# Performance work log

Hardware: AMD Instinct MI355X
Metric: run time of the kernel (lower is better)

The kernel has to match this reference:

```python
import jax, jax.numpy as jnp
import numpy as np

NH = 12      # attention heads
EPS = 1e-5   # torch nn.LayerNorm default


def _ln(x, g, b):
    m = jnp.mean(x, axis=-1, keepdims=True)
    v = jnp.var(x, axis=-1, keepdims=True)
    return (x - m) * jax.lax.rsqrt(v + EPS) * g + b


def _rel_table(table, n):
    # q_size == k_size == n, table length == 2n-1 -> pure gather, no interpolation
    idx = jnp.arange(n)[:, None] - jnp.arange(n)[None, :] + (n - 1)
    return table[idx]  # (n, n, head_dim)


def _attn2d(x, qkv_w, qkv_b, proj_w, proj_b, rel_h, rel_w):
    B, H, W, C = x.shape
    hd = C // NH
    scale = hd ** -0.5
    N = H * W
    qkv = x.reshape(B, N, C) @ qkv_w + qkv_b                    # (B, N, 3C)
    qkv = qkv.reshape(B, N, 3, NH, hd).transpose(2, 0, 3, 1, 4).reshape(3, B * NH, N, hd)
    q, k, v = qkv[0], qkv[1], qkv[2]
    attn = jnp.einsum('bnd,bmd->bnm', q * scale, k)             # (B*NH, N, N)
    Rh = _rel_table(rel_h, H)
    Rw = _rel_table(rel_w, W)
    rq = q.reshape(B * NH, H, W, hd)                            # unscaled q, as in torch
    bias_h = jnp.einsum('bhwc,hkc->bhwk', rq, Rh)
    bias_w = jnp.einsum('bhwc,wkc->bhwk', rq, Rw)
    attn = (attn.reshape(B * NH, H, W, H, W)
            + bias_h[:, :, :, :, None]
            + bias_w[:, :, :, None, :]).reshape(B * NH, N, N)
    attn = jax.nn.softmax(attn, axis=-1)
    out = (attn @ v).reshape(B, NH, H, W, hd).transpose(0, 2, 3, 1, 4).reshape(B, H, W, C)
    return out @ proj_w + proj_b


def _win_part(x, ws):
    B, H, W, C = x.shape
    ph = (ws - H % ws) % ws
    pw = (ws - W % ws) % ws
    x = jnp.pad(x, ((0, 0), (0, ph), (0, pw), (0, 0)))
    Hp, Wp = H + ph, W + pw
    x = x.reshape(B, Hp // ws, ws, Wp // ws, ws, C).transpose(0, 1, 3, 2, 4, 5)
    return x.reshape(-1, ws, ws, C), (Hp, Wp)


def _win_unpart(wins, ws, pad_hw, hw):
    Hp, Wp = pad_hw
    H, W = hw
    B = wins.shape[0] // (Hp * Wp // ws // ws)
    x = wins.reshape(B, Hp // ws, Wp // ws, ws, ws, -1).transpose(0, 1, 3, 2, 4, 5)
    x = x.reshape(B, Hp, Wp, -1)
    return x[:, :H, :W, :]


def _block(x, ws, ln1g, ln1b, qkvw, qkvb, projw, projb, relh, relw,
           ln2g, ln2b, mw1, mb1, mw2, mb2):
    shortcut = x
    x = _ln(x, ln1g, ln1b)
    if ws > 0:
        H, W = x.shape[1], x.shape[2]
        x, pad_hw = _win_part(x, ws)
    x = _attn2d(x, qkvw, qkvb, projw, projb, relh, relw)
    if ws > 0:
        x = _win_unpart(x, ws, pad_hw, (H, W))
    x = shortcut + x
    h = _ln(x, ln2g, ln2b)
    h = jax.nn.gelu(h @ mw1 + mb1, approximate=False) @ mw2 + mb2
    return x + h


def setup_inputs() -> dict:
    key = jax.random.key(0)
    def rnd(i, shape, s=0.02):
        return jax.random.normal(jax.random.fold_in(key, i), shape, jnp.float32) * s
    C, M, HD = 768, 3072, 64
    d = {
        'x': rnd(0, (1, 3, 1024, 1024), 1.0),
        'patch_w': rnd(1, (16, 16, 3, C)),
        'patch_b': rnd(2, (C,)),
        'pos_embed': rnd(3, (1, 64, 64, C)),
    }
    i = 4
    for s, L in (('1', 27), ('2', 127)):
        for name, shape in (('ln1g', (C,)), ('ln1b', (C,)), ('qkvw', (C, 3 * C)),
                            ('qkvb', (3 * C,)), ('projw', (C, C)), ('projb', (C,)),
                            ('relh', (L, HD)), ('relw', (L, HD)),
                            ('ln2g', (C,)), ('ln2b', (C,)),
                            ('mw1', (C, M)), ('mb1', (M,)), ('mw2', (M, C)), ('mb2', (C,))):
            d[name + s] = rnd(i, shape)
            i += 1
    for s in ('1', '2'):
        d['ln1g' + s] = d['ln1g' + s] + 1.0
        d['ln2g' + s] = d['ln2g' + s] + 1.0
    return d


def reference(x, patch_w, patch_b, pos_embed,
              ln1g1, ln1b1, qkvw1, qkvb1, projw1, projb1, relh1, relw1,
              ln2g1, ln2b1, mw11, mb11, mw21, mb21,
              ln1g2, ln1b2, qkvw2, qkvb2, projw2, projb2, relh2, relw2,
              ln2g2, ln2b2, mw12, mb12, mw22, mb22):
    # patch embed: 16x16 stride-16 conv, output NHWC (B, 64, 64, 768)
    feat = jax.lax.conv_general_dilated(
        x, patch_w, window_strides=(16, 16), padding='VALID',
        dimension_numbers=('NCHW', 'HWIO', 'NHWC'))
    feat = feat + patch_b + pos_embed
    feat = _block(feat, 14, ln1g1, ln1b1, qkvw1, qkvb1, projw1, projb1,
                  relh1, relw1, ln2g1, ln2b1, mw11, mb11, mw21, mb21)
    feat = _block(feat, 0, ln1g2, ln1b2, qkvw2, qkvb2, projw2, projb2,
                  relh2, relw2, ln2g2, ln2b2, mw12, mb12, mw22, mb22)
    return feat
```

## Files before the change

### kernel.cpp

```cpp
#include <hip/hip_runtime.h>


using u16 = unsigned short;
using u32 = unsigned int;
using short8  = __attribute__((ext_vector_type(8))) short;
using floatx4 = __attribute__((ext_vector_type(4))) float;

__device__ __forceinline__ float bfu2f(u16 u) { return __builtin_bit_cast(float, (u32)u << 16); }
__device__ __forceinline__ u16   f2bfu(float f) {
  u32 u = __builtin_bit_cast(u32, f);
  return (u16)((u + 0x7fffu + ((u >> 16) & 1u)) >> 16);
}
__device__ __forceinline__ u32 cvtpk_bf16(float a, float b) {
  u32 r; asm("v_cvt_pk_bf16_f32 %0, %1, %2" : "=v"(r) : "v"(a), "v"(b)); return r;
}
#define DIV14(x) (((x) * 4682) >> 16)
#define WAIT_VM0()   __builtin_amdgcn_s_waitcnt(0x3f70)
#define WAIT_LGKM0() __builtin_amdgcn_s_waitcnt(0xc07f)

__device__ __forceinline__ void gld_lds16(const u16* g, u16* l) {
  __builtin_amdgcn_global_load_lds(
      (const __attribute__((address_space(1))) u32*)g,
      (__attribute__((address_space(3))) u32*)l, 16, 0, 0);
}

__global__ __launch_bounds__(256) void detect_k(const u16* __restrict__ x, int* __restrict__ flag)
{
  __shared__ int tot;
  if (threadIdx.x == 0) tot = 0;
  __syncthreads();
  int cnt = 0;
  for (int i = threadIdx.x; i < 4096; i += 256) {
    int e = (x[2 * i] >> 7) & 0xFF;
    cnt += (e >= 100 && e <= 134) ? 1 : 0;
  }
  atomicAdd(&tot, cnt);
  __syncthreads();
  if (threadIdx.x == 0) *flag = (tot >= 2458) ? 1 : 0;
}

struct CvtEnt { const void* src; int n; int dstoff; };
struct CvtArgs { CvtEnt e[24]; int cnt; };

__global__ __launch_bounds__(256) void tobf_multi_k(CvtArgs a, u16* __restrict__ dst,
                                                    const int* __restrict__ flag)
{
  int gid = blockIdx.x * 256 + threadIdx.x;
  bool isbf = (*flag != 0);
  for (int t = 0; t < a.cnt; ++t)
    if (gid < a.e[t].n)
      dst[a.e[t].dstoff + gid] = isbf ? ((const u16*)a.e[t].src)[gid]
                                      : f2bfu(((const float*)a.e[t].src)[gid]);
}

__global__ __launch_bounds__(256) void tobf4_k(const void* __restrict__ src, u16* __restrict__ dst,
                                               int n4, const int* __restrict__ flag)
{
  int i = blockIdx.x * 256 + threadIdx.x;
  if (i >= n4) return;
  ushort4 o;
  if (*flag) o = ((const ushort4*)src)[i];
  else {
    float4 f = ((const float4*)src)[i];
    o.x = f2bfu(f.x); o.y = f2bfu(f.y); o.z = f2bfu(f.z); o.w = f2bfu(f.w);
  }
  ((ushort4*)dst)[i] = o;
}

__global__ __launch_bounds__(256) void cvt_out_k(const float* __restrict__ src,
                                                 void* __restrict__ dst,
                                                 const int* __restrict__ flag)
{
  int i = blockIdx.x * 256 + threadIdx.x;
  float4 v = ((const float4*)src)[i];
  if (*flag) {
    ushort4 o;
    o.x = f2bfu(v.x); o.y = f2bfu(v.y); o.z = f2bfu(v.z); o.w = f2bfu(v.w);
    ((ushort4*)dst)[i] = o;
  } else {
    ((float4*)dst)[i] = v;
  }
}

struct TJob { const void* src; int dstoff; int K; int N; int blk0; };
struct TArgs { TJob j[6]; int njobs; };

__global__ __launch_bounds__(256) void tobfT_multi_k(TArgs a, u16* __restrict__ wa,
                                                     const int* __restrict__ flag)
{
  __shared__ u16 t[64][65];
  const int bid = blockIdx.x;
  int ji = 0;
  #pragma unroll
  for (int q = 1; q < 6; ++q) if (q < a.njobs && bid >= a.j[q].blk0) ji = q;
  const void* src = a.j[ji].src;
  u16* dst = wa + a.j[ji].dstoff;
  const int K = a.j[ji].K, N = a.j[ji].N;
  const int local = bid - a.j[ji].blk0;
  const int nx = N >> 6;
  const int bx = local % nx, by = local / nx;
  const int n0 = bx * 64, k0 = by * 64;
  const int r = threadIdx.x >> 2, c = (threadIdx.x & 3) * 16;
  if (*flag) {
    const u16* s = (const u16*)src + (size_t)(k0 + r) * N + n0 + c;
    union { uint4 v[2]; u16 e[16]; } u;
    u.v[0] = *(const uint4*)s; u.v[1] = *(const uint4*)(s + 8);
    #pragma unroll
    for (int j = 0; j < 16; ++j) t[c + j][r] = u.e[j];
  } else {
    const float* s = (const float*)src + (size_t)(k0 + r) * N + n0 + c;
    #pragma unroll
    for (int j = 0; j < 16; ++j) t[c + j][r] = f2bfu(s[j]);
  }
  __syncthreads();
  union { uint4 v[2]; u16 e[16]; } o;
  #pragma unroll
  for (int j = 0; j < 16; ++j) o.e[j] = t[r][c + j];
  u16* d = dst + (size_t)(n0 + r) * K + k0 + c;
  *(uint4*)d = o.v[0]; *(uint4*)(d + 8) = o.v[1];
}

__global__ __launch_bounds__(256) void im2col_k(const void* __restrict__ xv, u16* __restrict__ a,
                                                const int* __restrict__ flag)
{
  int t = blockIdx.x, tid = threadIdx.x;
  int py = t >> 6, px = t & 63;
  int ky = tid >> 4, kx = tid & 15;
  size_t src = (size_t)(py * 16 + ky) * 1024 + px * 16 + kx;
  u16 v0, v1, v2;
  if (*flag) {
    const u16* x = (const u16*)xv;
    v0 = x[src]; v1 = x[src + 1048576]; v2 = x[src + 2097152];
  } else {
    const float* x = (const float*)xv;
    v0 = f2bfu(x[src]); v1 = f2bfu(x[src + 1048576]); v2 = f2bfu(x[src + 2097152]);
  }
  size_t dst = (size_t)t * 768 + tid * 3;
  a[dst] = v0; a[dst + 1] = v1; a[dst + 2] = v2;
}

__global__ __launch_bounds__(256) void ln_k(const float* __restrict__ x,
                                            const u16* __restrict__ g,
                                            const u16* __restrict__ b,
                                            u16* __restrict__ y)
{
  const int t = blockIdx.x, tid = threadIdx.x;
  const float* xp = x + (size_t)t * 768;
  float v0 = xp[tid], v1 = xp[tid + 256], v2 = xp[tid + 512];
  float s = v0 + v1 + v2;
  float q = v0 * v0 + v1 * v1 + v2 * v2;
  #pragma unroll
  for (int off = 32; off; off >>= 1) { s += __shfl_xor(s, off); q += __shfl_xor(q, off); }
  __shared__ float red[8];
  int wid = tid >> 6, lane = tid & 63;
  if (lane == 0) { red[wid] = s; red[4 + wid] = q; }
  __syncthreads();
  s = red[0] + red[1] + red[2] + red[3];
  q = red[4] + red[5] + red[6] + red[7];
  float mean = s * (1.f / 768.f);
  float var  = q * (1.f / 768.f) - mean * mean;
  float rstd = rsqrtf(var + 1e-5f);
  u16* yp = y + (size_t)t * 768;
  yp[tid]       = f2bfu((v0 - mean) * rstd * bfu2f(g[tid])       + bfu2f(b[tid]));
  yp[tid + 256] = f2bfu((v1 - mean) * rstd * bfu2f(g[tid + 256]) + bfu2f(b[tid + 256]));
  yp[tid + 512] = f2bfu((v2 - mean) * rstd * bfu2f(g[tid + 512]) + bfu2f(b[tid + 512]));
}

__global__ __launch_bounds__(256) void ln_win_k(const float* __restrict__ x,
                                                const u16* __restrict__ g,
                                                const u16* __restrict__ b,
                                                u16* __restrict__ wout)
{
  const int t = blockIdx.x, tid = threadIdx.x;
  const int win = t / 196, tok = t - win * 196;
  const int ty = DIV14(tok), tx = tok - 14 * ty;
  const int gy = (win / 5) * 14 + ty, gx = (win % 5) * 14 + tx;
  u16* yp = wout + (size_t)t * 768;
  if (gy >= 64 || gx >= 64) {
    yp[tid] = 0; yp[tid + 256] = 0; yp[tid + 512] = 0;
    return;
  }
  const float* xp = x + (size_t)(gy * 64 + gx) * 768;
  float v0 = xp[tid], v1 = xp[tid + 256], v2 = xp[tid + 512];
  float s = v0 + v1 + v2;
  float q = v0 * v0 + v1 * v1 + v2 * v2;
  #pragma unroll
  for (int off = 32; off; off >>= 1) { s += __shfl_xor(s, off); q += __shfl_xor(q, off); }
  __shared__ float red[8];
  int wid = tid >> 6, lane = tid & 63;
  if (lane == 0) { red[wid] = s; red[4 + wid] = q; }
  __syncthreads();
  s = red[0] + red[1] + red[2] + red[3];
  q = red[4] + red[5] + red[6] + red[7];
  float mean = s * (1.f / 768.f);
  float var  = q * (1.f / 768.f) - mean * mean;
  float rstd = rsqrtf(var + 1e-5f);
  yp[tid]       = f2bfu((v0 - mean) * rstd * bfu2f(g[tid])       + bfu2f(b[tid]));
  yp[tid + 256] = f2bfu((v1 - mean) * rstd * bfu2f(g[tid + 256]) + bfu2f(b[tid + 256]));
  yp[tid + 512] = f2bfu((v2 - mean) * rstd * bfu2f(g[tid + 512]) + bfu2f(b[tid + 512]));
}

enum { MODE_QKV = 1, MODE_GELU = 3, MODE_FEATA = 5, MODE_RESA = 6 };

template<int BN>
__global__ __launch_bounds__(256) void mgemm_k(
    const u16* __restrict__ A, const u16* __restrict__ Bt, const u16* __restrict__ bias,
    int M, int N, int K, int mode,
    float* __restrict__ outf, u16* __restrict__ outb,
    const float* __restrict__ res, const u16* __restrict__ pos,
    u16* __restrict__ qb, u16* __restrict__ kb, u16* __restrict__ vt, int TW, int TP,
    const int* __restrict__ flagp)
{
  constexpr int NWN = BN / 64, NWM = 4 / NWN;
  constexpr int WTM = 128 / NWM;
  constexpr int MS = WTM / 16, NS = 4;
  __shared__ __align__(16) u16 As[2][128 * 32];
  __shared__ __align__(16) u16 Bs[2][BN * 32];
  const int tid = threadIdx.x;
  const int wid = tid >> 6, lane = tid & 63;
  const int l15 = lane & 15, quad = lane >> 4;
  const int wm = wid / NWN, wn = wid % NWN;
  const int m0 = blockIdx.y * 128, n0 = blockIdx.x * BN;
  const int nz = (int)gridDim.z;
  const int kloc = K / nz;
  const int kbeg = blockIdx.z * kloc, kend = kbeg + kloc;
  const bool z0 = (blockIdx.z == 0);

  floatx4 acc[MS][NS];
  #pragma unroll
  for (int i = 0; i < MS; ++i)
    #pragma unroll
    for (int j = 0; j < NS; ++j) acc[i][j] = (floatx4){0.f, 0.f, 0.f, 0.f};

  const int sr = lane >> 2, sc = (lane & 3) * 8;
  const u16* ag0 = A + (size_t)min(m0 + wid * 32 + sr,      M - 1) * K + sc;
  const u16* ag1 = A + (size_t)min(m0 + wid * 32 + 16 + sr, M - 1) * K + sc;
  const u16 *bg0 = nullptr, *bg1 = nullptr;
  if constexpr (BN == 128) {
    bg0 = Bt + (size_t)(n0 + wid * 32 + sr) * K + sc;
    bg1 = Bt + (size_t)(n0 + wid * 32 + 16 + sr) * K + sc;
  } else {
    bg0 = Bt + (size_t)(n0 + wid * 16 + sr) * K + sc;
  }

  auto issue = [&](int buf, int k0) {
    gld_lds16(ag0 + k0, &As[buf][(wid * 32) * 32]);
    gld_lds16(ag1 + k0, &As[buf][(wid * 32 + 16) * 32]);
    if constexpr (BN == 128) {
      gld_lds16(bg0 + k0, &Bs[buf][(wid * 32) * 32]);
      gld_lds16(bg1 + k0, &Bs[buf][(wid * 32 + 16) * 32]);
    } else {
      gld_lds16(bg0 + k0, &Bs[buf][(wid * 16) * 32]);
    }
  };

  issue(0, kbeg);
  int bufi = 0;
  for (int k0 = kbeg; k0 < kend; k0 += 32, bufi ^= 1) {
    WAIT_VM0();
    __syncthreads();
    if (k0 + 32 < kend) issue(bufi ^ 1, k0 + 32);
    short8 af[MS], bf[NS];
    #pragma unroll
    for (int ms = 0; ms < MS; ++ms)
      af[ms] = *(const short8*)&As[bufi][(wm * WTM + ms * 16 + l15) * 32 + quad * 8];
    #pragma unroll
    for (int ns = 0; ns < NS; ++ns)
      bf[ns] = *(const short8*)&Bs[bufi][(wn * 64 + ns * 16 + l15) * 32 + quad * 8];
    #pragma unroll
    for (int ms = 0; ms < MS; ++ms)
      #pragma unroll
      for (int ns = 0; ns < NS; ++ns)
        acc[ms][ns] = __builtin_amdgcn_mfma_f32_16x16x32_bf16(af[ms], bf[ns], acc[ms][ns], 0, 0, 0);
  }

  #pragma unroll
  for (int ms = 0; ms < MS; ++ms) {
    const int gmb = m0 + wm * WTM + ms * 16 + quad * 4;
    #pragma unroll
    for (int ns = 0; ns < NS; ++ns) {
      const int gn = n0 + wn * 64 + ns * 16 + l15;
      const float bb = bfu2f(bias[gn]);
      if (mode == MODE_QKV) {
        const int s = gn / 768, nn = gn - s * 768, h = nn >> 6, d = nn & 63;
        #pragma unroll
        for (int r = 0; r < 4; ++r) {
          int gm = gmb + r; if (gm >= M) continue;
          float v = acc[ms][ns][r] + bb;
          int b = gm / TW, tok = gm - b * TW;
          size_t bh = (size_t)(b * 12 + h);
          if (s == 0)      qb[(bh * TP + tok) * 64 + d] = f2bfu(v);
          else if (s == 1) kb[(bh * TP + tok) * 64 + d] = f2bfu(v);
          else             vt[(bh * 64 + d) * TP + tok] = f2bfu(v);
        }
      } else if (mode == MODE_GELU) {
        #pragma unroll
        for (int r = 0; r < 4; ++r) {
          int gm = gmb + r; if (gm >= M) continue;
          size_t o = (size_t)gm * N + gn;
          float v = acc[ms][ns][r] + bb;
          outb[o] = f2bfu(0.5f * v * (1.f + erff(v * 0.70710678f)));
        }
      } else if (mode == MODE_FEATA) {
        #pragma unroll
        for (int r = 0; r < 4; ++r) {
          int gm = gmb + r; if (gm >= M) continue;
          size_t o = (size_t)gm * N + gn;
          float v = acc[ms][ns][r];
          if (z0) v += bb + bfu2f(pos[o]);
          unsafeAtomicAdd(&outf[o], v);
        }
      } else {
        #pragma unroll
        for (int r = 0; r < 4; ++r) {
          int gm = gmb + r; if (gm >= M) continue;
          size_t o = (size_t)gm * N + gn;
          float v = acc[ms][ns][r];
          if (z0) v += bb + res[o];
          unsafeAtomicAdd(&outf[o], v);
        }
      }
    }
  }
}

template<int NT, int NTP, int TD, bool WIN>
__global__ __launch_bounds__(256) void flash_k(
    const u16* __restrict__ qb, const u16* __restrict__ kb, const u16* __restrict__ vt,
    const u16* __restrict__ relh, const u16* __restrict__ relw,
    u16* __restrict__ outb)
{
  constexpr int NTAB = 2 * TD - 1;
  constexpr int KT = NTP >> 6;
  constexpr float L2E = 1.4426950408889634f;
  constexpr float SC2 = 0.125f * L2E;
  constexpr int RQ  = 0;
  constexpr int RK0 = 4096;
  constexpr int RK1 = 8192;
  constexpr int RV0 = 12288;
  constexpr int RV1 = 16384;
  constexpr int RG  = 20480;
  constexpr int GWWIN = RG + 64 * 34;
  constexpr int TOT = WIN ? (GWWIN + 64 * 34) : (RG + 64 * 66);
  __shared__ __align__(16) u16 lds[TOT];

  const int tid = threadIdx.x, wid = tid >> 6, lane = tid & 63;
  const int l15 = lane & 15, quad = lane >> 4;
  const int qt = blockIdx.x, bh = blockIdx.y;
  const int q0 = qt * 64;
  const size_t kvbase = (size_t)bh * NTP * 64;
  const size_t vbase  = (size_t)bh * 64 * NTP;
  const int myrow = wid * 16 + l15;

  auto swb = [](int row, int blk) { return row * 64 + (((blk ^ row) & 7) << 3); };

  {
    const int r = tid >> 2, cb = (tid & 3) * 2;
    const int tok = WIN ? (q0 + r) : min(q0 + r, NT - 1);
    const uint4* p = (const uint4*)(qb + kvbase + (size_t)tok * 64 + cb * 8);
    *(uint4*)&lds[RQ + swb(r, cb)]     = p[0];
    *(uint4*)&lds[RQ + swb(r, cb + 1)] = p[1];
  }
  __syncthreads();
  short8 qf[2];
  qf[0] = *(const short8*)&lds[RQ + swb(myrow, quad)];
  qf[1] = *(const short8*)&lds[RQ + swb(myrow, 4 + quad)];
  WAIT_LGKM0();

  auto stageRB = [&](const u16* tab, int rowoff, int maxrow) {
    const int r = tid >> 2, cb = (tid & 3) * 2;
    const int tr = min(rowoff + r, maxrow);
    const uint4* p = (const uint4*)(tab + (size_t)tr * 64 + cb * 8);
    *(uint4*)&lds[RV0 + swb(r, cb)]     = p[0];
    *(uint4*)&lds[RV0 + swb(r, cb + 1)] = p[1];
  };
  auto gpass = [&](int gbase, int gstride, int ncols) {
    for (int ns = 0; ns < ncols / 16; ++ns) {
      floatx4 g = (floatx4){0.f, 0.f, 0.f, 0.f};
      #pragma unroll
      for (int ks = 0; ks < 2; ++ks) {
        short8 b = *(const short8*)&lds[RV0 + swb(ns * 16 + l15, ks * 4 + quad)];
        g = __builtin_amdgcn_mfma_f32_16x16x32_bf16(qf[ks], b, g, 0, 0, 0);
      }
      #pragma unroll
      for (int r = 0; r < 4; ++r)
        lds[gbase + (wid * 16 + quad * 4 + r) * gstride + ns * 16 + l15] = f2bfu(g[r] * L2E);
    }
  };

  float gwv[4][4];
  if constexpr (!WIN) {
    stageRB(relh, qt, NTAB - 1);  __syncthreads();
    gpass(RG, 66, 64);
    __syncthreads();
    stageRB(relw, 0, NTAB - 1);   __syncthreads();
    gpass(RK0, 66, 64);
    #pragma unroll
    for (int kbi = 0; kbi < 4; ++kbi)
      #pragma unroll
      for (int r = 0; r < 4; ++r) {
        const int iw = myrow + 63 - (kbi * 16 + quad * 4 + r);
        if (iw < 64) gwv[kbi][r] = bfu2f(lds[RK0 + myrow * 66 + iw]);
      }
    WAIT_LGKM0();
    __syncthreads();
    stageRB(relw, 64, NTAB - 1);  __syncthreads();
    gpass(RK0, 66, 64);
    #pragma unroll
    for (int kbi = 0; kbi < 4; ++kbi)
      #pragma unroll
      for (int r = 0; r < 4; ++r) {
        const int iw = myrow + 63 - (kbi * 16 + quad * 4 + r);
        if (iw >= 64) gwv[kbi][r] = bfu2f(lds[RK0 + myrow * 66 + iw - 64]);
      }
    WAIT_LGKM0();
  } else {
    stageRB(relh, 0, NTAB - 1);  __syncthreads();
    gpass(RG, 34, 32);
    __syncthreads();
    stageRB(relw, 0, NTAB - 1);  __syncthreads();
    gpass(GWWIN, 34, 32);
  }

  const int srow = lane >> 3;
  const int scol = (((lane & 7) ^ srow) & 7) << 3;
  const u16* kp  = kb + kvbase + (size_t)(wid * 16 + srow) * 64 + scol;
  const u16* kp2 = kp + 512;
  const u16* vp  = vt + vbase  + (size_t)(wid * 16 + srow) * NTP + scol;
  const u16* vp2 = vp + (size_t)8 * NTP;
  u16* const kd0 = &lds[RK0 + wid * 1024];
  u16* const kd1 = &lds[RK1 + wid * 1024];
  u16* const vd0 = &lds[RV0 + wid * 1024];
  u16* const vd1 = &lds[RV1 + wid * 1024];
  auto issueKV = [&](int buf) {
    u16* kdb = buf ? kd1 : kd0;
    u16* vdb = buf ? vd1 : vd0;
    gld_lds16(kp,  kdb);
    gld_lds16(kp2, kdb + 512);
    gld_lds16(vp,  vdb);
    gld_lds16(vp2, vdb + 512);
    kp += 4096; kp2 += 4096; vp += 64; vp2 += 64;
  };

  float mI = -3e38f, lI = 0.f;
  floatx4 Oacc[4];
  #pragma unroll
  for (int d = 0; d < 4; ++d) Oacc[d] = (floatx4){0.f, 0.f, 0.f, 0.f};

  int qy = 0, qx = 0;
  if constexpr (WIN) {
    const int tok0 = q0 + myrow;
    qy = DIV14(tok0); qx = tok0 - 14 * qy;
  }

  auto body = [&](int RKb, int RVb, int kt) {
    floatx4 sacc[4];
    #pragma unroll
    for (int kbi = 0; kbi < 4; ++kbi) sacc[kbi] = (floatx4){0.f, 0.f, 0.f, 0.f};
    __builtin_amdgcn_s_setprio(1);
    #pragma unroll
    for (int ks = 0; ks < 2; ++ks)
      #pragma unroll
      for (int kbi = 0; kbi < 4; ++kbi) {
        short8 a = *(const short8*)&lds[RKb + swb(kbi * 16 + l15, ks * 4 + quad)];
        sacc[kbi] = __builtin_amdgcn_mfma_f32_16x16x32_bf16(a, qf[ks], sacc[kbi], 0, 0, 0);
      }
    __builtin_amdgcn_s_setprio(0);

    float sv[4][4];
    if constexpr (!WIN) {
      #pragma unroll
      for (int kbi = 0; kbi < 4; ++kbi)
        #pragma unroll
        for (int r = 0; r < 4; ++r)
          sv[kbi][r] = fmaf(SC2, sacc[kbi][r], gwv[kbi][r]);
    } else {
      #pragma unroll
      for (int kbi = 0; kbi < 4; ++kbi)
        #pragma unroll
        for (int r = 0; r < 4; ++r) {
          const int j = kt * 64 + kbi * 16 + quad * 4 + r;
          const int ky = DIV14(j), kx = j - 14 * ky;
          int ih = qy - ky + 13; ih = max(0, min(ih, 31));
          int iw = qx - kx + 13; iw = max(0, min(iw, 31));
          float s = SC2 * sacc[kbi][r] + bfu2f(lds[RG + myrow * 34 + ih])
                                       + bfu2f(lds[GWWIN + myrow * 34 + iw]);
          sv[kbi][r] = (j < NT) ? s : -1e30f;
        }
    }

    float rm;
    {
      float a0 = fmaxf(fmaxf(sv[0][0], sv[0][1]), fmaxf(sv[0][2], sv[0][3]));
      float a1 = fmaxf(fmaxf(sv[1][0], sv[1][1]), fmaxf(sv[1][2], sv[1][3]));
      float a2 = fmaxf(fmaxf(sv[2][0], sv[2][1]), fmaxf(sv[2][2], sv[2][3]));
      float a3 = fmaxf(fmaxf(sv[3][0], sv[3][1]), fmaxf(sv[3][2], sv[3][3]));
      rm = fmaxf(fmaxf(a0, a1), fmaxf(a2, a3));
    }
    rm = fmaxf(rm, __shfl_xor(rm, 16));
    rm = fmaxf(rm, __shfl_xor(rm, 32));
    float ghv = 0.f;
    if constexpr (!WIN) ghv = bfu2f(lds[RG + myrow * 66 + (63 - kt)]);
    const float mt = rm + ghv;
    const float mn = fmaxf(mI, mt);
    const float tt = mn - ghv;

    float rs = 0.f;
    u32 pk[8];
    #pragma unroll
    for (int kbi = 0; kbi < 4; ++kbi) {
      float p0 = __builtin_amdgcn_exp2f(sv[kbi][0] - tt);
      float p1 = __builtin_amdgcn_exp2f(sv[kbi][1] - tt);
      float p2 = __builtin_amdgcn_exp2f(sv[kbi][2] - tt);
      float p3 = __builtin_amdgcn_exp2f(sv[kbi][3] - tt);
      rs += (p0 + p1) + (p2 + p3);
      pk[2 * kbi]     = cvtpk_bf16(p0, p1);
      pk[2 * kbi + 1] = cvtpk_bf16(p2, p3);
    }

    #pragma unroll
    for (int kbi = 0; kbi < 4; ++kbi) {
      const int col = kbi * 16 + quad * 4;
      uint2 w2; w2.x = pk[2 * kbi]; w2.y = pk[2 * kbi + 1];
      *(uint2*)&lds[RQ + myrow * 64 + ((((col >> 3) ^ myrow) & 7) << 3) + (col & 7)] = w2;
    }

    const float al = __builtin_amdgcn_exp2f(mI - mn);
    if (__any(mt > mI)) {
      #pragma unroll
      for (int d = 0; d < 4; ++d) Oacc[d] *= al;
    }
    mI = mn;

    __builtin_amdgcn_s_setprio(1);
    #pragma unroll
    for (int ks = 0; ks < 2; ++ks) {
      short8 pb = *(const short8*)&lds[RQ + swb(myrow, ks * 4 + quad)];
      #pragma unroll
      for (int d = 0; d < 4; ++d) {
        short8 a = *(const short8*)&lds[RVb + swb(d * 16 + l15, ks * 4 + quad)];
        Oacc[d] = __builtin_amdgcn_mfma_f32_16x16x32_bf16(a, pb, Oacc[d], 0, 0, 0);
      }
    }
    __builtin_amdgcn_s_setprio(0);

    rs += __shfl_xor(rs, 16);
    rs += __shfl_xor(rs, 32);
    lI = fmaf(lI, al, rs);
  };

  __syncthreads();
  issueKV(0);
  for (int kt = 0; kt < KT; kt += 2) {
    WAIT_VM0();
    __syncthreads();
    if (kt + 1 < KT) issueKV(1);
    body(RK0, RV0, kt);
    WAIT_VM0();
    __syncthreads();
    if (kt + 2 < KT) issueKV(0);
    body(RK1, RV1, kt + 1);
  }

  const float rinv = 1.f / lI;
  const int tok = q0 + myrow;
  u32 ow[8];
  #pragma unroll
  for (int d = 0; d < 4; ++d) {
    ow[2 * d]     = cvtpk_bf16(Oacc[d][0] * rinv, Oacc[d][1] * rinv);
    ow[2 * d + 1] = cvtpk_bf16(Oacc[d][2] * rinv, Oacc[d][3] * rinv);
  }
  if constexpr (WIN) {
    if (tok < NT) {
      const int win = bh / 12, h = bh - win * 12;
      const int ty = DIV14(tok), tx = tok - 14 * ty;
      const int gy = (win / 5) * 14 + ty, gx = (win % 5) * 14 + tx;
      if (gy < 64 && gx < 64) {
        u16* op = outb + (size_t)(gy * 64 + gx) * 768 + h * 64;
        #pragma unroll
        for (int d = 0; d < 4; ++d)
          *(uint2*)(op + d * 16 + quad * 4) = make_uint2(ow[2 * d], ow[2 * d + 1]);
      }
    }
  } else {
    u16* op = outb + (size_t)tok * 768 + bh * 64;
    #pragma unroll
    for (int d = 0; d < 4; ++d)
      *(uint2*)(op + d * 16 + quad * 4) = make_uint2(ow[2 * d], ow[2 * d + 1]);
  }
}

extern "C" void kernel_launch(void* const* d_in, const int* in_sizes, int n_in,
                              void* d_out, int out_size, void* d_ws, size_t ws_size,
                              hipStream_t stream)
{
  const void* x      = d_in[0];
  const void* patchw = d_in[1];
  const void* patchb = d_in[2];
  const void* pos    = d_in[3];
  const void *ln1g1 = d_in[4],  *ln1b1 = d_in[5];
  const void *qkvw1 = d_in[6],  *qkvb1 = d_in[7];
  const void *projw1= d_in[8],  *projb1= d_in[9];
  const void *relh1 = d_in[10], *relw1 = d_in[11];
  const void *ln2g1 = d_in[12], *ln2b1 = d_in[13];
  const void *mw11  = d_in[14], *mb11  = d_in[15];
  const void *mw21  = d_in[16], *mb21  = d_in[17];
  const void *ln1g2 = d_in[18], *ln1b2 = d_in[19];
  const void *qkvw2 = d_in[20], *qkvb2 = d_in[21];
  const void *projw2= d_in[22], *projb2= d_in[23];
  const void *relh2 = d_in[24], *relw2 = d_in[25];
  const void *ln2g2 = d_in[26], *ln2b2 = d_in[27];
  const void *mw12  = d_in[28], *mb12  = d_in[29];
  const void *mw22  = d_in[30], *mb22  = d_in[31];

  char* w = (char*)d_ws;
  int*   FLAG = (int*)w;  w += 64;
  float* R0 = (float*)w;  w += 12582912;
  float* R1 = (float*)w;  w += 12582912;
  u16*   B0 = (u16*)w;    w += 6291456;
  u16*   Wb = (u16*)w;    w += 7526400;
  u16*   QB = (u16*)w;    w += 9830400;
  u16*   KB = (u16*)w;    w += 9830400;
  u16*   VT = (u16*)w;    w += 9830400;
  u16*   Hb = (u16*)w;    w += 25165824;
  u16*   WA = (u16*)w;    w += 15335424;
  u16*   POSb = (u16*)w;  w += 6291456;
  u16*   PRM = (u16*)w;   w += 106560;
  u16*   Ap = Hb;

  constexpr int WA_QKV = 0, WA_PROJ = 1769472, WA_M1 = 2359296, WA_M2 = 4718592,
                WA_PATCH = 7077888;
  constexpr int PRM_PATCHB = 0, PB1 = 768, PBLK = 26240, PB2 = 768 + PBLK;
  constexpr int O_QKVB = 0, O_PROJB = 2304, O_MB1 = 3072, O_MB2 = 6144,
                O_LN1G = 6912, O_LN1B = 7680, O_LN2G = 8448, O_LN2B = 9216,
                O_RELH = 9984, O_RELW = 18112;

  detect_k<<<1, 256, 0, stream>>>((const u16*)x, FLAG);
  CvtArgs ca; int kk = 0;
  auto add = [&](const void* s, int n, int off) { ca.e[kk].src = s; ca.e[kk].n = n; ca.e[kk].dstoff = off; ++kk; };
  add(patchb, 768, PRM_PATCHB);
  add(qkvb1, 2304, PB1 + O_QKVB); add(projb1, 768, PB1 + O_PROJB);
  add(mb11, 3072, PB1 + O_MB1);   add(mb21, 768, PB1 + O_MB2);
  add(ln1g1, 768, PB1 + O_LN1G);  add(ln1b1, 768, PB1 + O_LN1B);
  add(ln2g1, 768, PB1 + O_LN2G);  add(ln2b1, 768, PB1 + O_LN2B);
  add(relh1, 27 * 64, PB1 + O_RELH); add(relw1, 27 * 64, PB1 + O_RELW);
  add(qkvb2, 2304, PB2 + O_QKVB); add(projb2, 768, PB2 + O_PROJB);
  add(mb12, 3072, PB2 + O_MB1);   add(mb22, 768, PB2 + O_MB2);
  add(ln1g2, 768, PB2 + O_LN1G);  add(ln1b2, 768, PB2 + O_LN1B);
  add(ln2g2, 768, PB2 + O_LN2G);  add(ln2b2, 768, PB2 + O_LN2B);
  add(relh2, 127 * 64, PB2 + O_RELH); add(relw2, 127 * 64, PB2 + O_RELW);
  ca.cnt = kk;
  tobf_multi_k<<<32, 256, 0, stream>>>(ca, PRM, FLAG);
  tobf4_k<<<3072, 256, 0, stream>>>(pos, POSb, 786432, FLAG);

  {
    TArgs ta; int nb = 0, jn = 0;
    auto addT = [&](const void* s, int dstoff, int K, int N) {
      ta.j[jn] = { s, dstoff, K, N, nb }; nb += (N >> 6) * (K >> 6); ++jn;
    };
    addT(patchw, WA_PATCH, 768, 768);
    addT(qkvw1,  WA_QKV,   768, 2304);
    addT(projw1, WA_PROJ,  768, 768);
    addT(mw11,   WA_M1,    768, 3072);
    addT(mw21,   WA_M2,   3072, 768);
    ta.njobs = jn;
    tobfT_multi_k<<<nb, 256, 0, stream>>>(ta, WA, FLAG);
  }

  im2col_k<<<4096, 256, 0, stream>>>(x, Ap, FLAG);
  hipMemsetAsync(R0, 0, 12582912, stream);
  mgemm_k<64><<<dim3(12, 32, 2), 256, 0, stream>>>(Ap, WA + WA_PATCH, PRM + PRM_PATCHB,
      4096, 768, 768, MODE_FEATA, R0, nullptr, nullptr, POSb, nullptr, nullptr, nullptr, 0, 0, FLAG);

  ln_win_k<<<4900, 256, 0, stream>>>(R0, PRM + PB1 + O_LN1G, PRM + PB1 + O_LN1B, Wb);
  hipMemsetAsync(VT, 0, 9830400, stream);
  mgemm_k<128><<<dim3(18, 39), 256, 0, stream>>>(Wb, WA + WA_QKV, PRM + PB1 + O_QKVB,
      4900, 2304, 768, MODE_QKV, nullptr, nullptr, nullptr, nullptr, QB, KB, VT, 196, 256, FLAG);
  flash_k<196, 256, 14, true><<<dim3(4, 300), 256, 0, stream>>>(QB, KB, VT,
      PRM + PB1 + O_RELH, PRM + PB1 + O_RELW, B0);
  hipMemsetAsync(R1, 0, 12582912, stream);
  mgemm_k<64><<<dim3(12, 32, 2), 256, 0, stream>>>(B0, WA + WA_PROJ, PRM + PB1 + O_PROJB,
      4096, 768, 768, MODE_RESA, R1, nullptr, R0, nullptr, nullptr, nullptr, nullptr, 0, 0, FLAG);
  ln_k<<<4096, 256, 0, stream>>>(R1, PRM + PB1 + O_LN2G, PRM + PB1 + O_LN2B, B0);
  mgemm_k<128><<<dim3(24, 32), 256, 0, stream>>>(B0, WA + WA_M1, PRM + PB1 + O_MB1,
      4096, 3072, 768, MODE_GELU, nullptr, Hb, nullptr, nullptr, nullptr, nullptr, nullptr, 0, 0, FLAG);
  hipMemsetAsync(R0, 0, 12582912, stream);
  mgemm_k<64><<<dim3(12, 32, 2), 256, 0, stream>>>(Hb, WA + WA_M2, PRM + PB1 + O_MB2,
      4096, 768, 3072, MODE_RESA, R0, nullptr, R1, nullptr, nullptr, nullptr, nullptr, 0, 0, FLAG);

  {
    TArgs ta; int nb = 0, jn = 0;
    auto addT = [&](const void* s, int dstoff, int K, int N) {
      ta.j[jn] = { s, dstoff, K, N, nb }; nb += (N >> 6) * (K >> 6); ++jn;
    };
    addT(qkvw2,  WA_QKV,  768, 2304);
    addT(projw2, WA_PROJ, 768, 768);
    addT(mw12,   WA_M1,   768, 3072);
    addT(mw22,   WA_M2,  3072, 768);
    ta.njobs = jn;
    tobfT_multi_k<<<nb, 256, 0, stream>>>(ta, WA, FLAG);
  }

  ln_k<<<4096, 256, 0, stream>>>(R0, PRM + PB2 + O_LN1G, PRM + PB2 + O_LN1B, B0);
  mgemm_k<128><<<dim3(18, 32), 256, 0, stream>>>(B0, WA + WA_QKV, PRM + PB2 + O_QKVB,
      4096, 2304, 768, MODE_QKV, nullptr, nullptr, nullptr, nullptr, QB, KB, VT, 4096, 4096, FLAG);
  flash_k<4096, 4096, 64, false><<<dim3(64, 12), 256, 0, stream>>>(QB, KB, VT,
      PRM + PB2 + O_RELH, PRM + PB2 + O_RELW, B0);
  hipMemsetAsync(R1, 0, 12582912, stream);
  mgemm_k<64><<<dim3(12, 32, 2), 256, 0, stream>>>(B0, WA + WA_PROJ, PRM + PB2 + O_PROJB,
      4096, 768, 768, MODE_RESA, R1, nullptr, R0, nullptr, nullptr, nullptr, nullptr, 0, 0, FLAG);
  ln_k<<<4096, 256, 0, stream>>>(R1, PRM + PB2 + O_LN2G, PRM + PB2 + O_LN2B, B0);
  mgemm_k<128><<<dim3(24, 32), 256, 0, stream>>>(B0, WA + WA_M1, PRM + PB2 + O_MB1,
      4096, 3072, 768, MODE_GELU, nullptr, Hb, nullptr, nullptr, nullptr, nullptr, nullptr, 0, 0, FLAG);
  hipMemsetAsync(R0, 0, 12582912, stream);
  mgemm_k<64><<<dim3(12, 32, 2), 256, 0, stream>>>(Hb, WA + WA_M2, PRM + PB2 + O_MB2,
      4096, 768, 3072, MODE_RESA, R0, nullptr, R1, nullptr, nullptr, nullptr, nullptr, 0, 0, FLAG);
  cvt_out_k<<<3072, 256, 0, stream>>>(R0, d_out, FLAG);
}
```

Measured before the change: 788.8 us.

## Replace split-K atomic GEMMs with dedicated 64x64 swizzled-LDS GEMM kernel

Result: faster. 712.6 us (-9.7%).

```diff
diff --git a/kernel.cpp b/kernel.cpp
--- a/kernel.cpp
+++ b/kernel.cpp
@@ -65,21 +65,6 @@
     o.x = f2bfu(f.x); o.y = f2bfu(f.y); o.z = f2bfu(f.z); o.w = f2bfu(f.w);
   }
   ((ushort4*)dst)[i] = o;
-}
-
-__global__ __launch_bounds__(256) void cvt_out_k(const float* __restrict__ src,
-                                                 void* __restrict__ dst,
-                                                 const int* __restrict__ flag)
-{
-  int i = blockIdx.x * 256 + threadIdx.x;
-  float4 v = ((const float4*)src)[i];
-  if (*flag) {
-    ushort4 o;
-    o.x = f2bfu(v.x); o.y = f2bfu(v.y); o.z = f2bfu(v.z); o.w = f2bfu(v.w);
-    ((ushort4*)dst)[i] = o;
-  } else {
-    ((float4*)dst)[i] = v;
-  }
 }
 
 struct TJob { const void* src; int dstoff; int K; int N; int blk0; };
@@ -200,14 +185,89 @@
   yp[tid + 512] = f2bfu((v2 - mean) * rstd * bfu2f(g[tid + 512]) + bfu2f(b[tid + 512]));
 }
 
-enum { MODE_QKV = 1, MODE_GELU = 3, MODE_FEATA = 5, MODE_RESA = 6 };
+enum { MODE_FEAT = 0, MODE_QKV = 1, MODE_RES = 2, MODE_GELU = 3, MODE_OUT = 4 };
+
+__global__ __launch_bounds__(256) void mgemm64_k(
+    const u16* __restrict__ A, const u16* __restrict__ Bt, const u16* __restrict__ bias,
+    int N, int K, int mode,
+    float* __restrict__ outf, u16* __restrict__ outb,
+    const float* __restrict__ res, const u16* __restrict__ pos,
+    const int* __restrict__ flagp)
+{
+  __shared__ __align__(16) u16 As[2][64 * 64];
+  __shared__ __align__(16) u16 Bs[2][64 * 64];
+  const int tid = threadIdx.x;
+  const int wid = tid >> 6, lane = tid & 63;
+  const int l15 = lane & 15, quad = lane >> 4;
+  const int m0 = blockIdx.y * 64, n0 = blockIdx.x * 64;
+
+  auto swb = [](int row, int blk) { return row * 64 + (((blk ^ row) & 7) << 3); };
+
+  floatx4 acc[4];
+  #pragma unroll
+  for (int ns = 0; ns < 4; ++ns) acc[ns] = (floatx4){0.f, 0.f, 0.f, 0.f};
+
+  const int srow = lane >> 3;
+  const int scol = ((lane & 7) ^ srow) << 3;
+  const u16* ap0 = A  + (size_t)(m0 + wid * 16 + srow) * K + scol;
+  const u16* ap1 = ap0 + (size_t)8 * K;
+  const u16* bp0 = Bt + (size_t)(n0 + wid * 16 + srow) * K + scol;
+  const u16* bp1 = bp0 + (size_t)8 * K;
+
+  auto issue = [&](int buf, int k0) {
+    gld_lds16(ap0 + k0, &As[buf][(wid * 16) * 64]);
+    gld_lds16(ap1 + k0, &As[buf][(wid * 16 + 8) * 64]);
+    gld_lds16(bp0 + k0, &Bs[buf][(wid * 16) * 64]);
+    gld_lds16(bp1 + k0, &Bs[buf][(wid * 16 + 8) * 64]);
+  };
+
+  issue(0, 0);
+  int bufi = 0;
+  for (int k0 = 0; k0 < K; k0 += 64, bufi ^= 1) {
+    WAIT_VM0();
+    __syncthreads();
+    if (k0 + 64 < K) issue(bufi ^ 1, k0 + 64);
+    short8 af[2], bf[4][2];
+    af[0] = *(const short8*)&As[bufi][swb(wid * 16 + l15, quad)];
+    af[1] = *(const short8*)&As[bufi][swb(wid * 16 + l15, 4 + quad)];
+    #pragma unroll
+    for (int ns = 0; ns < 4; ++ns) {
+      bf[ns][0] = *(const short8*)&Bs[bufi][swb(ns * 16 + l15, quad)];
+      bf[ns][1] = *(const short8*)&Bs[bufi][swb(ns * 16 + l15, 4 + quad)];
+    }
+    #pragma unroll
+    for (int ns = 0; ns < 4; ++ns) {
+      acc[ns] = __builtin_amdgcn_mfma_f32_16x16x32_bf16(af[0], bf[ns][0], acc[ns], 0, 0, 0);
+      acc[ns] = __builtin_amdgcn_mfma_f32_16x16x32_bf16(af[1], bf[ns][1], acc[ns], 0, 0, 0);
+    }
+  }
+
+  const bool outbf = (mode == MODE_OUT) ? (*flagp != 0) : false;
+  const int gm0 = m0 + wid * 16 + quad * 4;
+  #pragma unroll
+  for (int ns = 0; ns < 4; ++ns) {
+    const int gn = n0 + ns * 16 + l15;
+    const float bb = bfu2f(bias[gn]);
+    #pragma unroll
+    for (int r = 0; r < 4; ++r) {
+      const size_t o = (size_t)(gm0 + r) * N + gn;
+      float v = acc[ns][r] + bb;
+      if (mode == MODE_FEAT)      outf[o] = v + bfu2f(pos[o]);
+      else if (mode == MODE_RES)  outf[o] = v + res[o];
+      else {
+        float ov = v + res[o];
+        if (outbf) outb[o] = f2bfu(ov);
+        else       outf[o] = ov;
+      }
+    }
+  }
+}
 
 template<int BN>
 __global__ __launch_bounds__(256) void mgemm_k(
     const u16* __restrict__ A, const u16* __restrict__ Bt, const u16* __restrict__ bias,
     int M, int N, int K, int mode,
-    float* __restrict__ outf, u16* __restrict__ outb,
-    const float* __restrict__ res, const u16* __restrict__ pos,
+    u16* __restrict__ outb,
     u16* __restrict__ qb, u16* __restrict__ kb, u16* __restrict__ vt, int TW, int TP,
     const int* __restrict__ flagp)
 {
@@ -221,10 +281,6 @@
   const int l15 = lane & 15, quad = lane >> 4;
   const int wm = wid / NWN, wn = wid % NWN;
   const int m0 = blockIdx.y * 128, n0 = blockIdx.x * BN;
-  const int nz = (int)gridDim.z;
-  const int kloc = K / nz;
-  const int kbeg = blockIdx.z * kloc, kend = kbeg + kloc;
-  const bool z0 = (blockIdx.z == 0);
 
   floatx4 acc[MS][NS];
   #pragma unroll
@@ -254,12 +310,12 @@
     }
   };
 
-  issue(0, kbeg);
+  issue(0, 0);
   int bufi = 0;
-  for (int k0 = kbeg; k0 < kend; k0 += 32, bufi ^= 1) {
+  for (int k0 = 0; k0 < K; k0 += 32, bufi ^= 1) {
     WAIT_VM0();
     __syncthreads();
-    if (k0 + 32 < kend) issue(bufi ^ 1, k0 + 32);
+    if (k0 + 32 < K) issue(bufi ^ 1, k0 + 32);
     short8 af[MS], bf[NS];
     #pragma unroll
     for (int ms = 0; ms < MS; ++ms)
@@ -293,31 +349,13 @@
           else if (s == 1) kb[(bh * TP + tok) * 64 + d] = f2bfu(v);
           else             vt[(bh * 64 + d) * TP + tok] = f2bfu(v);
         }
-      } else if (mode == MODE_GELU) {
+      } else {
         #pragma unroll
         for (int r = 0; r < 4; ++r) {
           int gm = gmb + r; if (gm >= M) continue;
           size_t o = (size_t)gm * N + gn;
           float v = acc[ms][ns][r] + bb;
           outb[o] = f2bfu(0.5f * v * (1.f + erff(v * 0.70710678f)));
-        }
-      } else if (mode == MODE_FEATA) {
-        #pragma unroll
-        for (int r = 0; r < 4; ++r) {
-          int gm = gmb + r; if (gm >= M) continue;
-          size_t o = (size_t)gm * N + gn;
-          float v = acc[ms][ns][r];
-          if (z0) v += bb + bfu2f(pos[o]);
-          unsafeAtomicAdd(&outf[o], v);
-        }
-      } else {
-        #pragma unroll
-        for (int r = 0; r < 4; ++r) {
-          int gm = gmb + r; if (gm >= M) continue;
-          size_t o = (size_t)gm * N + gn;
-          float v = acc[ms][ns][r];
-          if (z0) v += bb + res[o];
-          unsafeAtomicAdd(&outf[o], v);
         }
       }
     }
@@ -668,25 +706,22 @@
   }
 
   im2col_k<<<4096, 256, 0, stream>>>(x, Ap, FLAG);
-  hipMemsetAsync(R0, 0, 12582912, stream);
-  mgemm_k<64><<<dim3(12, 32, 2), 256, 0, stream>>>(Ap, WA + WA_PATCH, PRM + PRM_PATCHB,
-      4096, 768, 768, MODE_FEATA, R0, nullptr, nullptr, POSb, nullptr, nullptr, nullptr, 0, 0, FLAG);
+  mgemm64_k<<<dim3(12, 64), 256, 0, stream>>>(Ap, WA + WA_PATCH, PRM + PRM_PATCHB,
+      768, 768, MODE_FEAT, R0, nullptr, nullptr, POSb, FLAG);
 
   ln_win_k<<<4900, 256, 0, stream>>>(R0, PRM + PB1 + O_LN1G, PRM + PB1 + O_LN1B, Wb);
   hipMemsetAsync(VT, 0, 9830400, stream);
   mgemm_k<128><<<dim3(18, 39), 256, 0, stream>>>(Wb, WA + WA_QKV, PRM + PB1 + O_QKVB,
-      4900, 2304, 768, MODE_QKV, nullptr, nullptr, nullptr, nullptr, QB, KB, VT, 196, 256, FLAG);
+      4900, 2304, 768, MODE_QKV, nullptr, QB, KB, VT, 196, 256, FLAG);
   flash_k<196, 256, 14, true><<<dim3(4, 300), 256, 0, stream>>>(QB, KB, VT,
       PRM + PB1 + O_RELH, PRM + PB1 + O_RELW, B0);
-  hipMemsetAsync(R1, 0, 12582912, stream);
-  mgemm_k<64><<<dim3(12, 32, 2), 256, 0, stream>>>(B0, WA + WA_PROJ, PRM + PB1 + O_PROJB,
-      4096, 768, 768, MODE_RESA, R1, nullptr, R0, nullptr, nullptr, nullptr, nullptr, 0, 0, FLAG);
+  mgemm64_k<<<dim3(12, 64), 256, 0, stream>>>(B0, WA + WA_PROJ, PRM + PB1 + O_PROJB,
+      768, 768, MODE_RES, R1, nullptr, R0, nullptr, FLAG);
   ln_k<<<4096, 256, 0, stream>>>(R1, PRM + PB1 + O_LN2G, PRM + PB1 + O_LN2B, B0);
   mgemm_k<128><<<dim3(24, 32), 256, 0, stream>>>(B0, WA + WA_M1, PRM + PB1 + O_MB1,
-      4096, 3072, 768, MODE_GELU, nullptr, Hb, nullptr, nullptr, nullptr, nullptr, nullptr, 0, 0, FLAG);
-  hipMemsetAsync(R0, 0, 12582912, stream);
-  mgemm_k<64><<<dim3(12, 32, 2), 256, 0, stream>>>(Hb, WA + WA_M2, PRM + PB1 + O_MB2,
-      4096, 768, 3072, MODE_RESA, R0, nullptr, R1, nullptr, nullptr, nullptr, nullptr, 0, 0, FLAG);
+      4096, 3072, 768, MODE_GELU, Hb, nullptr, nullptr, nullptr, 0, 0, FLAG);
+  mgemm64_k<<<dim3(12, 64), 256, 0, stream>>>(Hb, WA + WA_M2, PRM + PB1 + O_MB2,
+      768, 3072, MODE_RES, R0, nullptr, R1, nullptr, FLAG);
 
   {
     TArgs ta; int nb = 0, jn = 0;
@@ -703,17 +738,14 @@
 
   ln_k<<<4096, 256, 0, stream>>>(R0, PRM + PB2 + O_LN1G, PRM + PB2 + O_LN1B, B0);
   mgemm_k<128><<<dim3(18, 32), 256, 0, stream>>>(B0, WA + WA_QKV, PRM + PB2 + O_QKVB,
-      4096, 2304, 768, MODE_QKV, nullptr, nullptr, nullptr, nullptr, QB, KB, VT, 4096, 4096, FLAG);
+      4096, 2304, 768, MODE_QKV, nullptr, QB, KB, VT, 4096, 4096, FLAG);
   flash_k<4096, 4096, 64, false><<<dim3(64, 12), 256, 0, stream>>>(QB, KB, VT,
       PRM + PB2 + O_RELH, PRM + PB2 + O_RELW, B0);
-  hipMemsetAsync(R1, 0, 12582912, stream);
-  mgemm_k<64><<<dim3(12, 32, 2), 256, 0, stream>>>(B0, WA + WA_PROJ, PRM + PB2 + O_PROJB,
-      4096, 768, 768, MODE_RESA, R1, nullptr, R0, nullptr, nullptr, nullptr, nullptr, 0, 0, FLAG);
+  mgemm64_k<<<dim3(12, 64), 256, 0, stream>>>(B0, WA + WA_PROJ, PRM + PB2 + O_PROJB,
+      768, 768, MODE_RES, R1, nullptr, R0, nullptr, FLAG);
   ln_k<<<4096, 256, 0, stream>>>(R1, PRM + PB2 + O_LN2G, PRM + PB2 + O_LN2B, B0);
   mgemm_k<128><<<dim3(24, 32), 256, 0, stream>>>(B0, WA + WA_M1, PRM + PB2 + O_MB1,
-      4096, 3072, 768, MODE_GELU, nullptr, Hb, nullptr, nullptr, nullptr, nullptr, nullptr, 0, 0, FLAG);
-  hipMemsetAsync(R0, 0, 12582912, stream);
-  mgemm_k<64><<<dim3(12, 32, 2), 256, 0, stream>>>(Hb, WA + WA_M2, PRM + PB2 + O_MB2,
-      4096, 768, 3072, MODE_RESA, R0, nullptr, R1, nullptr, nullptr, nullptr, nullptr, 0, 0, FLAG);
-  cvt_out_k<<<3072, 256, 0, stream>>>(R0, d_out, FLAG);
-}
+      4096, 3072, 768, MODE_GELU, Hb, nullptr, nullptr, nullptr, 0, 0, FLAG);
+  mgemm64_k<<<dim3(12, 64), 256, 0, stream>>>(Hb, WA + WA_M2, PRM + PB2 + O_MB2,
+      768, 3072, MODE_OUT, (float*)d_out, (u16*)d_out, R1, nullptr, FLAG);
+}
```
